# Kernel optimization log

Measured on AMD Instinct MI355X. Metric: run time of the kernel, lower is better.

## Reference

```python
import jax, jax.numpy as jnp
import numpy as np

LN_EPS = 1e-5

def sin_emb(coords, dim):
    # coords [..., 3] -> [..., dim]; dim split evenly over 3 axes, sin/cos halves
    per_axis = dim // 3
    half = per_axis // 2
    freqs = jnp.exp(-jnp.log(10000.0) * jnp.arange(half, dtype=coords.dtype) / max(half - 1, 1))
    ang = coords[..., None] * freqs  # [..., 3, half]
    emb = jnp.concatenate([jnp.sin(ang), jnp.cos(ang)], axis=-1)  # [..., 3, per_axis]
    return emb.reshape(coords.shape[:-1] + (dim,))

def layernorm(x, g, b):
    mu = jnp.mean(x, axis=-1, keepdims=True)
    var = jnp.mean((x - mu) ** 2, axis=-1, keepdims=True)
    return (x - mu) * jax.lax.rsqrt(var + LN_EPS) * g + b

def point_mlp(x, w, b, g, be, act):
    h = layernorm(x @ w + b, g, be)
    return jax.nn.gelu(h, approximate=False) if act else h

def query_ball_point(radius, nsample, xyz):
    # xyz [B,N,3] -> idx [B,N,nsample] (pad with first in-ball index, PointNet++ style)
    N = xyz.shape[1]
    sq = jnp.sum((xyz[:, :, None, :] - xyz[:, None, :, :]) ** 2, axis=-1)  # [B,N,N]
    idx0 = jnp.where(sq > radius * radius, N, jnp.arange(N)[None, None, :])
    idx = jnp.sort(idx0, axis=-1)[:, :, :nsample]
    return jnp.where(idx == N, idx[:, :, :1], idx)

def index_points(points, idx):
    # points [B,N,C], idx [B,S,K] -> [B,S,K,C]
    return jax.vmap(lambda p, i: p[i])(points, idx)

def setup_inputs() -> dict:
    key = jax.random.key(0)
    ks = jax.random.split(key, 20)
    B, N, C_stem, C_tok = 4, 4096, 64, 256
    C_in = C_stem + 3 + 24 + 96  # 187
    w = lambda k, i, o: jax.random.normal(k, (i, o), jnp.float32) * 0.02
    inp = {
        'xyz': jax.random.uniform(ks[0], (B, N, 3), jnp.float32),
        'point_feature': jax.random.normal(ks[1], (B, N, C_stem), jnp.float32),
        # scene_point_mlp
        'w1': w(ks[2], C_in, C_tok), 'b1': jnp.zeros((C_tok,)), 'g1': jnp.ones((C_tok,)), 'be1': jnp.zeros((C_tok,)),
        'w2': w(ks[3], C_tok, C_tok), 'b2': jnp.zeros((C_tok,)), 'g2': jnp.ones((C_tok,)), 'be2': jnp.zeros((C_tok,)),
        # scene_projection
        'pw1': w(ks[4], C_tok, C_tok), 'pb1': jnp.zeros((C_tok,)), 'pg1': jnp.ones((C_tok,)), 'pbe1': jnp.zeros((C_tok,)),
        'pw2': w(ks[5], C_tok, C_tok), 'pb2': jnp.zeros((C_tok,)), 'pg2': jnp.ones((C_tok,)), 'pbe2': jnp.zeros((C_tok,)),
    }
    return inp

def reference(xyz, point_feature, w1, b1, g1, be1, w2, b2, g2, be2,
              pw1, pb1, pg1, pbe1, pw2, pb2, pg2, pbe2):
    radius, K = 0.16, 32
    idx = query_ball_point(radius, K, xyz)                     # [B,N,K]
    grouped_xyz = index_points(xyz, idx)                       # [B,N,K,3]
    grouped_feature = index_points(point_feature, idx)         # [B,N,K,Cs]
    relative_xyz = grouped_xyz - xyz[:, :, None, :]            # [B,N,K,3]
    relative_position = sin_emb(relative_xyz, 24)              # [B,N,K,24]
    absolute_position = sin_emb(xyz, 96)                       # [B,N,96]
    B, N = xyz.shape[0], xyz.shape[1]
    absolute_position = jnp.broadcast_to(absolute_position[:, :, None, :], (B, N, K, 96))
    grouped_input = jnp.concatenate(
        (grouped_feature, relative_xyz, relative_position, absolute_position), axis=-1)
    h = point_mlp(grouped_input, w1, b1, g1, be1, True)
    h = point_mlp(h, w2, b2, g2, be2, False)
    scene_point_feature = jnp.max(h, axis=2)                   # [B,N,C]
    pooled = jnp.max(scene_point_feature, axis=1, keepdims=True)  # [B,1,C]
    t = point_mlp(pooled, pw1, pb1, pg1, pbe1, True)
    global_scene_token = point_mlp(t, pw2, pb2, pg2, pbe2, False)
    return global_scene_token
```

## Files before the change

### kernel.cpp

```cpp
#include <hip/hip_runtime.h>
#include <hip/hip_bf16.h>
#include <math.h>


#define LN_EPS 1e-5f

typedef __attribute__((ext_vector_type(8))) short bf16x8;
typedef __attribute__((ext_vector_type(4))) float f32x4;
typedef __attribute__((ext_vector_type(2))) unsigned int u32x2;
typedef __attribute__((ext_vector_type(4))) unsigned int u32x4;

#if __has_builtin(__builtin_amdgcn_rcpf)
#define FRCP(x) __builtin_amdgcn_rcpf(x)
#else
#define FRCP(x) (1.0f / (x))
#endif

__device__ __forceinline__ unsigned short f2bf(float f) {
    unsigned int x = __float_as_uint(f);
    return (unsigned short)((x + 0x7FFFu + ((x >> 16) & 1u)) >> 16);
}
__device__ __forceinline__ unsigned int pack2(float a, float b) {
    union { __hip_bfloat162 h; unsigned int u; } cvt;
    cvt.h = __float22bfloat162_rn(make_float2(a, b));
    return cvt.u;
}
__device__ __forceinline__ unsigned int fenc(float f) {
    unsigned int u = __float_as_uint(f);
    return (u & 0x80000000u) ? ~u : (u | 0x80000000u);
}
__device__ __forceinline__ float fdec(unsigned int u) {
    return __uint_as_float((u & 0x80000000u) ? (u & 0x7FFFFFFFu) : ~u);
}
__device__ __forceinline__ float gelu_fast(float x) {
    float x2 = x * x;
    float u = x * fmaf(0.0356774081f, x2, 0.7978845608f);
    float e = exp2f(u * -2.8853900818f);
    float r = FRCP(e + 1.0f);
    return x * r;
}
template<int CTRL>
__device__ __forceinline__ float dppadd(float s) {
    int v = __builtin_amdgcn_update_dpp(0, __float_as_int(s), CTRL, 0xF, 0xF, true);
    return s + __int_as_float(v);
}
__device__ __forceinline__ float rowsum16(float x) {
    x = dppadd<0x128>(x);
    x = dppadd<0x124>(x);
    x = dppadd<0x122>(x);
    x = dppadd<0x121>(x);
    return x;
}

__global__ __launch_bounds__(256) void k_prep(
    const float* __restrict__ w1, const float* __restrict__ w2,
    unsigned short* __restrict__ w2T, unsigned short* __restrict__ w1T,
    unsigned int* __restrict__ pooled, int* __restrict__ done)
{
    int t = threadIdx.x, blk = blockIdx.x;
    if (blk < 16) {
        __shared__ unsigned short tile[64][65];
        int tr = blk >> 2, tc = blk & 3;
        #pragma unroll
        for (int rr = 0; rr < 16; ++rr) {
            int kl = rr * 4 + (t >> 6), nl = t & 63;
            tile[kl][nl] = f2bf(w2[(size_t)(tr * 64 + kl) * 256 + tc * 64 + nl]);
        }
        __syncthreads();
        #pragma unroll
        for (int rr = 0; rr < 16; ++rr) {
            int nl = rr * 4 + (t >> 6), kp = t & 63;
            int kl = (kp & 3) * 16 + (kp >> 2);
            w2T[(size_t)(tc * 64 + nl) * 256 + tr * 64 + kp] = tile[kl][nl];
        }
    } else if (blk < 28) {
        __shared__ unsigned short tile[64][65];
        int idx = blk - 16;
        int tr = idx >> 2, tc = idx & 3;
        #pragma unroll
        for (int rr = 0; rr < 16; ++rr) {
            int kl = rr * 4 + (t >> 6), nl = t & 63;
            int kp = tr * 64 + kl;
            float v = 0.f;
            if (kp < 91)                       v = w1[(size_t)kp * 256 + tc * 64 + nl];
            else if (kp >= 92 && kp <= 187)    v = w1[(size_t)(kp - 1) * 256 + tc * 64 + nl];
            tile[kl][nl] = f2bf(v);
        }
        __syncthreads();
        #pragma unroll
        for (int rr = 0; rr < 16; ++rr) {
            int nl = rr * 4 + (t >> 6), kl = t & 63;
            w1T[(size_t)(tc * 64 + nl) * 192 + tr * 64 + kl] = tile[kl][nl];
        }
    } else {
        unsigned int idv = fenc(-1e19f);
        for (int q = t; q < 1024; q += 256) pooled[q] = idv;
        if (t == 0) *done = 0;
    }
}

__global__ __launch_bounds__(256, 4) void k_main(
    const float* __restrict__ xyz, const float* __restrict__ pf,
    const unsigned short* __restrict__ w1T, const unsigned short* __restrict__ w2T,
    const float* __restrict__ b1, const float* __restrict__ g1,
    const float* __restrict__ be1,
    const float* __restrict__ b2, const float* __restrict__ g2,
    const float* __restrict__ be2,
    unsigned int* __restrict__ pooled, int* __restrict__ done,
    const float* __restrict__ pw1, const float* __restrict__ pb1,
    const float* __restrict__ pg1, const float* __restrict__ pbe1,
    const float* __restrict__ pw2, const float* __restrict__ pb2,
    const float* __restrict__ pg2, const float* __restrict__ pbe2,
    float* __restrict__ out)
{
    __shared__ __align__(16) unsigned short smem[64 * 264];
    __shared__ __align__(16) unsigned int epack[2 * 48];
    __shared__ unsigned long long bmask[2][64];
    __shared__ int   idxs[64];
    __shared__ float ctr[2][3];
    __shared__ int   lastf;
    unsigned short* a1s = smem;
    unsigned short* h1s = smem;

    const int N = 4096;
    int tid = threadIdx.x, wv = tid >> 6, lane = tid & 63;
    int lo16 = lane & 15, quad = lane >> 4;
    int b = blockIdx.x & 3;
    int i0 = (blockIdx.x >> 2) * 2;
    size_t base = (size_t)b * N;
    const float* xb = xyz + base * 3;

    bf16x8 bfr0[4], bfr1[4];
    #pragma unroll
    for (int nt = 0; nt < 4; ++nt) {
        int n = wv * 64 + nt * 16 + lo16;
        bfr0[nt] = *(const bf16x8*)&w1T[n * 192 + 0 * 32 + quad * 8];
        bfr1[nt] = *(const bf16x8*)&w1T[n * 192 + 1 * 32 + quad * 8];
    }

    if (tid < 6) { int p = tid / 3, a = tid - 3 * p; ctr[p][a] = xb[(i0 + p) * 3 + a]; }
    if (tid < 96) {
        int p = tid / 48, pr = tid - 48 * p;
        float vals[2];
        #pragma unroll
        for (int q = 0; q < 2; ++q) {
            int cc = pr * 2 + q;
            int a = cc >> 5, wI = cc & 31;
            int jf = (wI < 16) ? wI : (wI - 16);
            float coord = xb[(i0 + p) * 3 + a];
            float fr = __expf(-0.61402269146507894f * (float)jf);
            float ang = coord * fr;
            vals[q] = (wI < 16) ? __sinf(ang) : __cosf(ang);
        }
        epack[p * 48 + pr] = pack2(vals[0], vals[1]);
    }
    const double r2d = 0.16 * 0.16;
    float T = (float)r2d;
    if ((double)T > r2d) T = __uint_as_float(__float_as_uint(T) - 1u);
    {
        float cx0 = xb[i0 * 3], cy0 = xb[i0 * 3 + 1], cz0 = xb[i0 * 3 + 2];
        float cx1 = xb[(i0 + 1) * 3], cy1 = xb[(i0 + 1) * 3 + 1], cz1 = xb[(i0 + 1) * 3 + 2];
        #pragma unroll 4
        for (int i = 0; i < 16; ++i) {
            int chunk = wv * 16 + i;
            int j = chunk * 64 + lane;
            float px = xb[j * 3], py = xb[j * 3 + 1], pz = xb[j * 3 + 2];
            float dx0 = __fsub_rn(px, cx0), dy0 = __fsub_rn(py, cy0), dz0 = __fsub_rn(pz, cz0);
            float sq0 = __fadd_rn(__fadd_rn(__fmul_rn(dx0, dx0), __fmul_rn(dy0, dy0)),
                                  __fmul_rn(dz0, dz0));
            unsigned long long m0 = __ballot(sq0 <= T);
            float dx1 = __fsub_rn(px, cx1), dy1 = __fsub_rn(py, cy1), dz1 = __fsub_rn(pz, cz1);
            float sq1 = __fadd_rn(__fadd_rn(__fmul_rn(dx1, dx1), __fmul_rn(dy1, dy1)),
                                  __fmul_rn(dz1, dz1));
            unsigned long long m1 = __ballot(sq1 <= T);
            if (lane == 0) { bmask[0][chunk] = m0; bmask[1][chunk] = m1; }
        }
    }
    __syncthreads();
    if (wv < 2) {
        int p = wv;
        unsigned long long m = bmask[p][lane];
        int c = __popcll(m);
        int inc = c;
        #pragma unroll
        for (int d = 1; d <= 32; d <<= 1) {
            int v = __shfl_up(inc, d);
            if (lane >= d) inc += v;
        }
        int exc = inc - c;
        int total = __shfl(inc, 63);
        unsigned long long lm = __ballot(m != 0ull);
        int fl = __ffsll(lm) - 1;
        unsigned long long mf = (unsigned long long)__shfl((long long)m, fl);
        int firstj = fl * 64 + __ffsll(mf) - 1;
        unsigned long long mm = m;
        int t = 0;
        while (mm != 0ull && (exc + t) < 32) {
            int bpos = __ffsll(mm) - 1;
            idxs[p * 32 + exc + t] = lane * 64 + bpos;
            mm &= mm - 1; ++t;
        }
        if (lane >= total && lane < 32) idxs[p * 32 + lane] = firstj;
    }
    __syncthreads();

    {
        int r = tid >> 2, seg = tid & 3;
        int j = idxs[r];
        const f32x4* src = (const f32x4*)(pf + (base + (size_t)j) * 64 + seg * 16);
        f32x4 v0 = src[0], v1 = src[1], v2 = src[2], v3 = src[3];
        u32x4 o0, o1;
        o0.x = pack2(v0.x, v0.y); o0.y = pack2(v0.z, v0.w);
        o0.z = pack2(v1.x, v1.y); o0.w = pack2(v1.z, v1.w);
        o1.x = pack2(v2.x, v2.y); o1.y = pack2(v2.z, v2.w);
        o1.z = pack2(v3.x, v3.y); o1.w = pack2(v3.z, v3.w);
        u32x4* dst = (u32x4*)&a1s[r * 200 + seg * 16];
        dst[0] = o0; dst[1] = o1;
    }
    {
        int r = tid & 63, part = tid >> 6;
        int p = r >> 5;
        int j = idxs[r];
        float rx = xb[j * 3]     - ctr[p][0];
        float ry = xb[j * 3 + 1] - ctr[p][1];
        float rz = xb[j * 3 + 2] - ctr[p][2];
        unsigned short* arow = &a1s[r * 200];
        if (part == 0) {
            *(unsigned int*)&arow[64] = pack2(rx, ry);
            arow[66] = f2bf(rz);
            arow[91] = 0;
            *(u32x2*)&arow[188] = (u32x2){0u, 0u};
        } else {
            int a = part - 1;
            float cv = (a == 0) ? rx : ((a == 1) ? ry : rz);
            const float fr4[4] = {1.f, 0.046415888336127774f,
                                  0.0021544346900318843f, 1e-4f};
            float sn[4], cs[4];
            #pragma unroll
            for (int tt = 0; tt < 4; ++tt) {
                float ang = cv * fr4[tt];
                sn[tt] = __sinf(ang); cs[tt] = __cosf(ang);
            }
            arow[67 + a * 8 + 0] = f2bf(sn[0]); arow[67 + a * 8 + 1] = f2bf(sn[1]);
            arow[67 + a * 8 + 2] = f2bf(sn[2]); arow[67 + a * 8 + 3] = f2bf(sn[3]);
            arow[67 + a * 8 + 4] = f2bf(cs[0]); arow[67 + a * 8 + 5] = f2bf(cs[1]);
            arow[67 + a * 8 + 6] = f2bf(cs[2]); arow[67 + a * 8 + 7] = f2bf(cs[3]);
        }
    }
    {
        int r = tid >> 2, part = tid & 3, p = r >> 5;
        const u32x2* e = (const u32x2*)(epack + p * 48 + part * 12);
        u32x2* dst = (u32x2*)&a1s[r * 200 + 92 + part * 24];
        #pragma unroll
        for (int q = 0; q < 6; ++q) dst[q] = e[q];
    }
    __syncthreads();

    f32x4 acc[4][4];
    {
        float b1f[4];
        #pragma unroll
        for (int nt = 0; nt < 4; ++nt) b1f[nt] = b1[wv * 64 + nt * 16 + lo16];
        #pragma unroll
        for (int mt = 0; mt < 4; ++mt)
            #pragma unroll
            for (int nt = 0; nt < 4; ++nt)
                #pragma unroll
                for (int reg = 0; reg < 4; ++reg) acc[mt][nt][reg] = b1f[nt];
    }
    #pragma unroll
    for (int mt = 0; mt < 4; ++mt) {
        bf16x8 afr = *(const bf16x8*)&a1s[(mt * 16 + lo16) * 200 + 0 * 32 + quad * 8];
        #pragma unroll
        for (int nt = 0; nt < 4; ++nt)
            acc[mt][nt] = __builtin_amdgcn_mfma_f32_16x16x32_bf16(
                afr, bfr0[nt], acc[mt][nt], 0, 0, 0);
    }
    #pragma unroll
    for (int mt = 0; mt < 4; ++mt) {
        bf16x8 afr = *(const bf16x8*)&a1s[(mt * 16 + lo16) * 200 + 1 * 32 + quad * 8];
        #pragma unroll
        for (int nt = 0; nt < 4; ++nt)
            acc[mt][nt] = __builtin_amdgcn_mfma_f32_16x16x32_bf16(
                afr, bfr1[nt], acc[mt][nt], 0, 0, 0);
    }
    for (int ks = 2; ks < 6; ++ks) {
        bf16x8 bfr[4];
        #pragma unroll
        for (int nt = 0; nt < 4; ++nt) {
            int n = wv * 64 + nt * 16 + lo16;
            bfr[nt] = *(const bf16x8*)&w1T[n * 192 + ks * 32 + quad * 8];
        }
        #pragma unroll
        for (int mt = 0; mt < 4; ++mt) {
            bf16x8 afr = *(const bf16x8*)&a1s[(mt * 16 + lo16) * 200 + ks * 32 + quad * 8];
            #pragma unroll
            for (int nt = 0; nt < 4; ++nt)
                acc[mt][nt] = __builtin_amdgcn_mfma_f32_16x16x32_bf16(
                    afr, bfr[nt], acc[mt][nt], 0, 0, 0);
        }
    }

    __shared__ float reds[64][4][2];
    __shared__ float musig[64][2];
    #pragma unroll
    for (int mt = 0; mt < 4; ++mt) {
        #pragma unroll
        for (int reg = 0; reg < 4; ++reg) {
            float s1 = 0.f, s2 = 0.f;
            #pragma unroll
            for (int nt = 0; nt < 4; ++nt) { float v = acc[mt][nt][reg]; s1 += v; s2 = fmaf(v, v, s2); }
            s1 = rowsum16(s1); s2 = rowsum16(s2);
            if (lo16 == 0) { int r = mt * 16 + quad * 4 + reg; reds[r][wv][0] = s1; reds[r][wv][1] = s2; }
        }
    }
    __syncthreads();
    if (tid < 64) {
        int r = tid;
        float s1 = reds[r][0][0] + reds[r][1][0] + reds[r][2][0] + reds[r][3][0];
        float s2 = reds[r][0][1] + reds[r][1][1] + reds[r][2][1] + reds[r][3][1];
        float mu = s1 * (1.f / 256.f);
        float var = fmaxf(s2 * (1.f / 256.f) - mu * mu, 0.f);
        musig[r][0] = mu; musig[r][1] = rsqrtf(var + LN_EPS);
    }
    __syncthreads();
    {
        float g1f[4], be1f[4];
        #pragma unroll
        for (int nt = 0; nt < 4; ++nt) {
            int n = wv * 64 + nt * 16 + lo16;
            g1f[nt] = g1[n]; be1f[nt] = be1[n];
        }
        #pragma unroll
        for (int mt = 0; mt < 4; ++mt) {
            #pragma unroll
            for (int reg = 0; reg < 4; ++reg) {
                int r = mt * 16 + quad * 4 + reg;
                float mu = musig[r][0], rs = musig[r][1];
                float v0 = gelu_fast(fmaf((acc[mt][0][reg] - mu) * rs, g1f[0], be1f[0]));
                float v1 = gelu_fast(fmaf((acc[mt][1][reg] - mu) * rs, g1f[1], be1f[1]));
                float v2 = gelu_fast(fmaf((acc[mt][2][reg] - mu) * rs, g1f[2], be1f[2]));
                float v3 = gelu_fast(fmaf((acc[mt][3][reg] - mu) * rs, g1f[3], be1f[3]));
                u32x2 w; w.x = pack2(v0, v1); w.y = pack2(v2, v3);
                *(u32x2*)&h1s[r * 264 + wv * 64 + lo16 * 4] = w;
            }
        }
    }
    __syncthreads();

    {
        float b2f[4];
        #pragma unroll
        for (int nt = 0; nt < 4; ++nt) b2f[nt] = b2[wv * 64 + nt * 16 + lo16];
        #pragma unroll
        for (int mt = 0; mt < 4; ++mt)
            #pragma unroll
            for (int nt = 0; nt < 4; ++nt)
                #pragma unroll
                for (int reg = 0; reg < 4; ++reg) acc[mt][nt][reg] = b2f[nt];
    }
    for (int ks = 0; ks < 8; ++ks) {
        bf16x8 bfr[4], afr[4];
        #pragma unroll
        for (int nt = 0; nt < 4; ++nt) {
            int n = wv * 64 + nt * 16 + lo16;
            bfr[nt] = *(const bf16x8*)&w2T[n * 256 + ks * 32 + quad * 8];
        }
        #pragma unroll
        for (int mt = 0; mt < 4; ++mt)
            afr[mt] = *(const bf16x8*)&h1s[(mt * 16 + lo16) * 264 + ks * 32 + quad * 8];
        #pragma unroll
        for (int mt = 0; mt < 4; ++mt)
            #pragma unroll
            for (int nt = 0; nt < 4; ++nt)
                acc[mt][nt] = __builtin_amdgcn_mfma_f32_16x16x32_bf16(
                    afr[mt], bfr[nt], acc[mt][nt], 0, 0, 0);
    }

    {
        #pragma unroll
        for (int mt = 0; mt < 4; ++mt) {
            #pragma unroll
            for (int reg = 0; reg < 4; ++reg) {
                float s1 = 0.f, s2 = 0.f;
                #pragma unroll
                for (int nt = 0; nt < 4; ++nt) { float v = acc[mt][nt][reg]; s1 += v; s2 = fmaf(v, v, s2); }
                s1 = rowsum16(s1); s2 = rowsum16(s2);
                if (lo16 == 0) { int r = mt * 16 + quad * 4 + reg; reds[r][wv][0] = s1; reds[r][wv][1] = s2; }
            }
        }
        __syncthreads();
        if (tid < 64) {
            int r = tid;
            float s1 = reds[r][0][0] + reds[r][1][0] + reds[r][2][0] + reds[r][3][0];
            float s2 = reds[r][0][1] + reds[r][1][1] + reds[r][2][1] + reds[r][3][1];
            float mu = s1 * (1.f / 256.f);
            float var = fmaxf(s2 * (1.f / 256.f) - mu * mu, 0.f);
            musig[r][0] = mu; musig[r][1] = rsqrtf(var + LN_EPS);
        }
        __syncthreads();

        float g2f[4], be2f[4];
        #pragma unroll
        for (int nt = 0; nt < 4; ++nt) {
            int n = wv * 64 + nt * 16 + lo16;
            g2f[nt] = g2[n]; be2f[nt] = be2[n];
        }
        float mx[4] = {-1e30f, -1e30f, -1e30f, -1e30f};
        #pragma unroll
        for (int mt = 0; mt < 4; ++mt) {
            #pragma unroll
            for (int reg = 0; reg < 4; ++reg) {
                int r = mt * 16 + quad * 4 + reg;
                float mu = musig[r][0], rs = musig[r][1];
                #pragma unroll
                for (int nt = 0; nt < 4; ++nt) {
                    float v = fmaf((acc[mt][nt][reg] - mu) * rs, g2f[nt], be2f[nt]);
                    mx[nt] = fmaxf(mx[nt], v);
                }
            }
        }
        #pragma unroll
        for (int nt = 0; nt < 4; ++nt) {
            mx[nt] = fmaxf(mx[nt], __shfl_xor(mx[nt], 16));
            mx[nt] = fmaxf(mx[nt], __shfl_xor(mx[nt], 32));
        }
        if (quad == 0) {
            #pragma unroll
            for (int nt = 0; nt < 4; ++nt)
                atomicMax(pooled + b * 256 + wv * 64 + nt * 16 + lo16, fenc(mx[nt]));
        }
    }

    __syncthreads();
    if (tid == 0) lastf = (atomicAdd(done, 1) == 8191);
    __syncthreads();
    if (!lastf) return;
    {
        int bb = wv;
        float* xw = (float*)smem + wv * 512;
        #pragma unroll
        for (int q = 0; q < 4; ++q)
            xw[q * 64 + lane] =
                fdec(atomicMax(&pooled[bb * 256 + q * 64 + lane], 0u));

        float a1[4];
        #pragma unroll
        for (int q = 0; q < 4; ++q) a1[q] = pb1[q * 64 + lane];
        #pragma unroll 4
        for (int k = 0; k < 256; ++k) {
            float xv = xw[k];
            const float* wr = pw1 + (size_t)k * 256 + lane;
            #pragma unroll
            for (int q = 0; q < 4; ++q) a1[q] = fmaf(xv, wr[q * 64], a1[q]);
        }
        float s1 = a1[0] + a1[1] + a1[2] + a1[3];
        float s2 = fmaf(a1[0], a1[0], fmaf(a1[1], a1[1],
                   fmaf(a1[2], a1[2], a1[3] * a1[3])));
        s1 = rowsum16(s1); s2 = rowsum16(s2);
        s1 += __shfl_xor(s1, 16); s2 += __shfl_xor(s2, 16);
        s1 += __shfl_xor(s1, 32); s2 += __shfl_xor(s2, 32);
        float mu = s1 * (1.f / 256.f);
        float rs = rsqrtf(fmaxf(s2 * (1.f / 256.f) - mu * mu, 0.f) + LN_EPS);
        #pragma unroll
        for (int q = 0; q < 4; ++q) {
            int c = q * 64 + lane;
            xw[256 + c] = gelu_fast(fmaf((a1[q] - mu) * rs, pg1[c], pbe1[c]));
        }

        float a2[4];
        #pragma unroll
        for (int q = 0; q < 4; ++q) a2[q] = pb2[q * 64 + lane];
        #pragma unroll 4
        for (int k = 0; k < 256; ++k) {
            float xv = xw[256 + k];
            const float* wr = pw2 + (size_t)k * 256 + lane;
            #pragma unroll
            for (int q = 0; q < 4; ++q) a2[q] = fmaf(xv, wr[q * 64], a2[q]);
        }
        s1 = a2[0] + a2[1] + a2[2] + a2[3];
        s2 = fmaf(a2[0], a2[0], fmaf(a2[1], a2[1],
             fmaf(a2[2], a2[2], a2[3] * a2[3])));
        s1 = rowsum16(s1); s2 = rowsum16(s2);
        s1 += __shfl_xor(s1, 16); s2 += __shfl_xor(s2, 16);
        s1 += __shfl_xor(s1, 32); s2 += __shfl_xor(s2, 32);
        mu = s1 * (1.f / 256.f);
        rs = rsqrtf(fmaxf(s2 * (1.f / 256.f) - mu * mu, 0.f) + LN_EPS);
        #pragma unroll
        for (int q = 0; q < 4; ++q) {
            int c = q * 64 + lane;
            out[bb * 256 + c] = fmaf((a2[q] - mu) * rs, pg2[c], pbe2[c]);
        }
    }
}

extern "C" void kernel_launch(void* const* d_in, const int* in_sizes, int n_in,
                              void* d_out, int out_size, void* d_ws, size_t ws_size,
                              hipStream_t stream)
{
    char* ws = (char*)d_ws;
    unsigned short* w2T    = (unsigned short*)ws;
    unsigned short* w1T    = (unsigned short*)(ws + (128u << 10));
    unsigned int*   pooled = (unsigned int*)(ws + (224u << 10));
    int*            done   = (int*)(ws + (228u << 10));

    k_prep<<<29, 256, 0, stream>>>((const float*)d_in[2], (const float*)d_in[6],
                                   w2T, w1T, pooled, done);
    k_main<<<8192, 256, 0, stream>>>((const float*)d_in[0], (const float*)d_in[1],
                                     w1T, w2T,
                                     (const float*)d_in[3], (const float*)d_in[4],
                                     (const float*)d_in[5],
                                     (const float*)d_in[7], (const float*)d_in[8],
                                     (const float*)d_in[9], pooled, done,
                                     (const float*)d_in[10], (const float*)d_in[11],
                                     (const float*)d_in[12], (const float*)d_in[13],
                                     (const float*)d_in[14], (const float*)d_in[15],
                                     (const float*)d_in[16], (const float*)d_in[17],
                                     (float*)d_out);
}
```

Baseline: 418.9 us.

## Process four centers per block with 512 threads and a 2x4 wave grid

Each block now handles four query points (128 grouped rows) with 8 waves arranged as 2 M-groups by 4 N-groups, halving the grid to 4096 blocks. The ball query computes four ballots per loaded point, and center coordinates are read with vector loads. Fewer blocks means fewer repeated weight-fragment loads, fewer per-block setup scans over all 4096 points, and fewer atomics per center. The cost is that shared memory roughly doubles to about 70KB per block, which limits occupancy, and the per-block scan still reads every point for only four centers.

```diff
diff --git a/kernel.cpp b/kernel.cpp
--- a/kernel.cpp
+++ b/kernel.cpp
@@ -99,7 +99,7 @@
     }
 }
 
-__global__ __launch_bounds__(256, 4) void k_main(
+__global__ __launch_bounds__(512, 4) void k_main(
     const float* __restrict__ xyz, const float* __restrict__ pf,
     const unsigned short* __restrict__ w1T, const unsigned short* __restrict__ w2T,
     const float* __restrict__ b1, const float* __restrict__ g1,
@@ -113,11 +113,11 @@
     const float* __restrict__ pg2, const float* __restrict__ pbe2,
     float* __restrict__ out)
 {
-    __shared__ __align__(16) unsigned short smem[64 * 264];
-    __shared__ __align__(16) unsigned int epack[2 * 48];
-    __shared__ unsigned long long bmask[2][64];
-    __shared__ int   idxs[64];
-    __shared__ float ctr[2][3];
+    __shared__ __align__(16) unsigned short smem[128 * 264];
+    __shared__ __align__(16) unsigned int epack[4 * 48];
+    __shared__ unsigned long long bmask[4][64];
+    __shared__ int   idxs[128];
+    __shared__ float ctr[4][3];
     __shared__ int   lastf;
     unsigned short* a1s = smem;
     unsigned short* h1s = smem;
@@ -125,21 +125,21 @@
     const int N = 4096;
     int tid = threadIdx.x, wv = tid >> 6, lane = tid & 63;
     int lo16 = lane & 15, quad = lane >> 4;
+    int wvM = wv >> 2, wvN = wv & 3;
     int b = blockIdx.x & 3;
-    int i0 = (blockIdx.x >> 2) * 2;
+    int i0 = (blockIdx.x >> 2) * 4;
     size_t base = (size_t)b * N;
     const float* xb = xyz + base * 3;
 
-    bf16x8 bfr0[4], bfr1[4];
+    bf16x8 bfr0[4];
     #pragma unroll
     for (int nt = 0; nt < 4; ++nt) {
-        int n = wv * 64 + nt * 16 + lo16;
+        int n = wvN * 64 + nt * 16 + lo16;
         bfr0[nt] = *(const bf16x8*)&w1T[n * 192 + 0 * 32 + quad * 8];
-        bfr1[nt] = *(const bf16x8*)&w1T[n * 192 + 1 * 32 + quad * 8];
-    }
-
-    if (tid < 6) { int p = tid / 3, a = tid - 3 * p; ctr[p][a] = xb[(i0 + p) * 3 + a]; }
-    if (tid < 96) {
+    }
+
+    if (tid < 12) { int p = tid / 3, a = tid - 3 * p; ctr[p][a] = xb[(i0 + p) * 3 + a]; }
+    if (tid < 192) {
         int p = tid / 48, pr = tid - 48 * p;
         float vals[2];
         #pragma unroll
@@ -158,13 +158,19 @@
     float T = (float)r2d;
     if ((double)T > r2d) T = __uint_as_float(__float_as_uint(T) - 1u);
     {
-        float cx0 = xb[i0 * 3], cy0 = xb[i0 * 3 + 1], cz0 = xb[i0 * 3 + 2];
-        float cx1 = xb[(i0 + 1) * 3], cy1 = xb[(i0 + 1) * 3 + 1], cz1 = xb[(i0 + 1) * 3 + 2];
-        #pragma unroll 4
-        for (int i = 0; i < 16; ++i) {
-            int chunk = wv * 16 + i;
+        f32x4 cA = *(const f32x4*)(xb + (size_t)i0 * 3);
+        f32x4 cB = *(const f32x4*)(xb + (size_t)i0 * 3 + 4);
+        f32x4 cC = *(const f32x4*)(xb + (size_t)i0 * 3 + 8);
+        float cx0 = cA.x, cy0 = cA.y, cz0 = cA.z;
+        float cx1 = cA.w, cy1 = cB.x, cz1 = cB.y;
+        float cx2 = cB.z, cy2 = cB.w, cz2 = cC.x;
+        float cx3 = cC.y, cy3 = cC.z, cz3 = cC.w;
+        #pragma unroll 2
+        for (int i = 0; i < 8; ++i) {
+            int chunk = wv * 8 + i;
             int j = chunk * 64 + lane;
-            float px = xb[j * 3], py = xb[j * 3 + 1], pz = xb[j * 3 + 2];
+            const float* pp = xb + (size_t)j * 3;
+            float px = pp[0], py = pp[1], pz = pp[2];
             float dx0 = __fsub_rn(px, cx0), dy0 = __fsub_rn(py, cy0), dz0 = __fsub_rn(pz, cz0);
             float sq0 = __fadd_rn(__fadd_rn(__fmul_rn(dx0, dx0), __fmul_rn(dy0, dy0)),
                                   __fmul_rn(dz0, dz0));
@@ -173,11 +179,22 @@
             float sq1 = __fadd_rn(__fadd_rn(__fmul_rn(dx1, dx1), __fmul_rn(dy1, dy1)),
                                   __fmul_rn(dz1, dz1));
             unsigned long long m1 = __ballot(sq1 <= T);
-            if (lane == 0) { bmask[0][chunk] = m0; bmask[1][chunk] = m1; }
-        }
-    }
-    __syncthreads();
-    if (wv < 2) {
+            float dx2 = __fsub_rn(px, cx2), dy2 = __fsub_rn(py, cy2), dz2 = __fsub_rn(pz, cz2);
+            float sq2 = __fadd_rn(__fadd_rn(__fmul_rn(dx2, dx2), __fmul_rn(dy2, dy2)),
+                                  __fmul_rn(dz2, dz2));
+            unsigned long long m2 = __ballot(sq2 <= T);
+            float dx3 = __fsub_rn(px, cx3), dy3 = __fsub_rn(py, cy3), dz3 = __fsub_rn(pz, cz3);
+            float sq3 = __fadd_rn(__fadd_rn(__fmul_rn(dx3, dx3), __fmul_rn(dy3, dy3)),
+                                  __fmul_rn(dz3, dz3));
+            unsigned long long m3 = __ballot(sq3 <= T);
+            if (lane == 0) {
+                bmask[0][chunk] = m0; bmask[1][chunk] = m1;
+                bmask[2][chunk] = m2; bmask[3][chunk] = m3;
+            }
+        }
+    }
+    __syncthreads();
+    if (wv < 4) {
         int p = wv;
         unsigned long long m = bmask[p][lane];
         int c = __popcll(m);
@@ -218,7 +235,7 @@
         dst[0] = o0; dst[1] = o1;
     }
     {
-        int r = tid & 63, part = tid >> 6;
+        int r = tid & 127, part = tid >> 7;
         int p = r >> 5;
         int j = idxs[r];
         float rx = xb[j * 3]     - ctr[p][0];
@@ -254,13 +271,20 @@
         #pragma unroll
         for (int q = 0; q < 6; ++q) dst[q] = e[q];
     }
-    __syncthreads();
-
+    bf16x8 bfr1[4];
+    #pragma unroll
+    for (int nt = 0; nt < 4; ++nt) {
+        int n = wvN * 64 + nt * 16 + lo16;
+        bfr1[nt] = *(const bf16x8*)&w1T[n * 192 + 1 * 32 + quad * 8];
+    }
+    __syncthreads();
+
+    const int arow0 = wvM * 64;
     f32x4 acc[4][4];
     {
         float b1f[4];
         #pragma unroll
-        for (int nt = 0; nt < 4; ++nt) b1f[nt] = b1[wv * 64 + nt * 16 + lo16];
+        for (int nt = 0; nt < 4; ++nt) b1f[nt] = b1[wvN * 64 + nt * 16 + lo16];
         #pragma unroll
         for (int mt = 0; mt < 4; ++mt)
             #pragma unroll
@@ -270,7 +294,7 @@
     }
     #pragma unroll
     for (int mt = 0; mt < 4; ++mt) {
-        bf16x8 afr = *(const bf16x8*)&a1s[(mt * 16 + lo16) * 200 + 0 * 32 + quad * 8];
+        bf16x8 afr = *(const bf16x8*)&a1s[(arow0 + mt * 16 + lo16) * 200 + 0 * 32 + quad * 8];
         #pragma unroll
         for (int nt = 0; nt < 4; ++nt)
             acc[mt][nt] = __builtin_amdgcn_mfma_f32_16x16x32_bf16(
@@ -278,7 +302,7 @@
     }
     #pragma unroll
     for (int mt = 0; mt < 4; ++mt) {
-        bf16x8 afr = *(const bf16x8*)&a1s[(mt * 16 + lo16) * 200 + 1 * 32 + quad * 8];
+        bf16x8 afr = *(const bf16x8*)&a1s[(arow0 + mt * 16 + lo16) * 200 + 1 * 32 + quad * 8];
         #pragma unroll
         for (int nt = 0; nt < 4; ++nt)
             acc[mt][nt] = __builtin_amdgcn_mfma_f32_16x16x32_bf16(
@@ -288,12 +312,12 @@
         bf16x8 bfr[4];
         #pragma unroll
         for (int nt = 0; nt < 4; ++nt) {
-            int n = wv * 64 + nt * 16 + lo16;
+            int n = wvN * 64 + nt * 16 + lo16;
             bfr[nt] = *(const bf16x8*)&w1T[n * 192 + ks * 32 + quad * 8];
         }
         #pragma unroll
         for (int mt = 0; mt < 4; ++mt) {
-            bf16x8 afr = *(const bf16x8*)&a1s[(mt * 16 + lo16) * 200 + ks * 32 + quad * 8];
+            bf16x8 afr = *(const bf16x8*)&a1s[(arow0 + mt * 16 + lo16) * 200 + ks * 32 + quad * 8];
             #pragma unroll
             for (int nt = 0; nt < 4; ++nt)
                 acc[mt][nt] = __builtin_amdgcn_mfma_f32_16x16x32_bf16(
@@ -301,8 +325,8 @@
         }
     }
 
-    __shared__ float reds[64][4][2];
-    __shared__ float musig[64][2];
+    __shared__ float reds[128][4][2];
+    __shared__ float musig[128][2];
     #pragma unroll
     for (int mt = 0; mt < 4; ++mt) {
         #pragma unroll
@@ -311,11 +335,14 @@
             #pragma unroll
             for (int nt = 0; nt < 4; ++nt) { float v = acc[mt][nt][reg]; s1 += v; s2 = fmaf(v, v, s2); }
             s1 = rowsum16(s1); s2 = rowsum16(s2);
-            if (lo16 == 0) { int r = mt * 16 + quad * 4 + reg; reds[r][wv][0] = s1; reds[r][wv][1] = s2; }
-        }
-    }
-    __syncthreads();
-    if (tid < 64) {
+            if (lo16 == 0) {
+                int r = arow0 + mt * 16 + quad * 4 + reg;
+                reds[r][wvN][0] = s1; reds[r][wvN][1] = s2;
+            }
+        }
+    }
+    __syncthreads();
+    if (tid < 128) {
         int r = tid;
         float s1 = reds[r][0][0] + reds[r][1][0] + reds[r][2][0] + reds[r][3][0];
         float s2 = reds[r][0][1] + reds[r][1][1] + reds[r][2][1] + reds[r][3][1];
@@ -328,21 +355,21 @@
         float g1f[4], be1f[4];
         #pragma unroll
         for (int nt = 0; nt < 4; ++nt) {
-            int n = wv * 64 + nt * 16 + lo16;
+            int n = wvN * 64 + nt * 16 + lo16;
             g1f[nt] = g1[n]; be1f[nt] = be1[n];
         }
         #pragma unroll
         for (int mt = 0; mt < 4; ++mt) {
             #pragma unroll
             for (int reg = 0; reg < 4; ++reg) {
-                int r = mt * 16 + quad * 4 + reg;
+                int r = arow0 + mt * 16 + quad * 4 + reg;
                 float mu = musig[r][0], rs = musig[r][1];
                 float v0 = gelu_fast(fmaf((acc[mt][0][reg] - mu) * rs, g1f[0], be1f[0]));
                 float v1 = gelu_fast(fmaf((acc[mt][1][reg] - mu) * rs, g1f[1], be1f[1]));
                 float v2 = gelu_fast(fmaf((acc[mt][2][reg] - mu) * rs, g1f[2], be1f[2]));
                 float v3 = gelu_fast(fmaf((acc[mt][3][reg] - mu) * rs, g1f[3], be1f[3]));
                 u32x2 w; w.x = pack2(v0, v1); w.y = pack2(v2, v3);
-                *(u32x2*)&h1s[r * 264 + wv * 64 + lo16 * 4] = w;
+                *(u32x2*)&h1s[r * 264 + wvN * 64 + lo16 * 4] = w;
             }
         }
     }
@@ -351,7 +378,7 @@
     {
         float b2f[4];
         #pragma unroll
-        for (int nt = 0; nt < 4; ++nt) b2f[nt] = b2[wv * 64 + nt * 16 + lo16];
+        for (int nt = 0; nt < 4; ++nt) b2f[nt] = b2[wvN * 64 + nt * 16 + lo16];
         #pragma unroll
         for (int mt = 0; mt < 4; ++mt)
             #pragma unroll
@@ -363,12 +390,12 @@
         bf16x8 bfr[4], afr[4];
         #pragma unroll
         for (int nt = 0; nt < 4; ++nt) {
-            int n = wv * 64 + nt * 16 + lo16;
+            int n = wvN * 64 + nt * 16 + lo16;
             bfr[nt] = *(const bf16x8*)&w2T[n * 256 + ks * 32 + quad * 8];
         }
         #pragma unroll
         for (int mt = 0; mt < 4; ++mt)
-            afr[mt] = *(const bf16x8*)&h1s[(mt * 16 + lo16) * 264 + ks * 32 + quad * 8];
+            afr[mt] = *(const bf16x8*)&h1s[(arow0 + mt * 16 + lo16) * 264 + ks * 32 + quad * 8];
         #pragma unroll
         for (int mt = 0; mt < 4; ++mt)
             #pragma unroll
@@ -386,11 +413,14 @@
                 #pragma unroll
                 for (int nt = 0; nt < 4; ++nt) { float v = acc[mt][nt][reg]; s1 += v; s2 = fmaf(v, v, s2); }
                 s1 = rowsum16(s1); s2 = rowsum16(s2);
-                if (lo16 == 0) { int r = mt * 16 + quad * 4 + reg; reds[r][wv][0] = s1; reds[r][wv][1] = s2; }
+                if (lo16 == 0) {
+                    int r = arow0 + mt * 16 + quad * 4 + reg;
+                    reds[r][wvN][0] = s1; reds[r][wvN][1] = s2;
+                }
             }
         }
         __syncthreads();
-        if (tid < 64) {
+        if (tid < 128) {
             int r = tid;
             float s1 = reds[r][0][0] + reds[r][1][0] + reds[r][2][0] + reds[r][3][0];
             float s2 = reds[r][0][1] + reds[r][1][1] + reds[r][2][1] + reds[r][3][1];
@@ -403,7 +433,7 @@
         float g2f[4], be2f[4];
         #pragma unroll
         for (int nt = 0; nt < 4; ++nt) {
-            int n = wv * 64 + nt * 16 + lo16;
+            int n = wvN * 64 + nt * 16 + lo16;
             g2f[nt] = g2[n]; be2f[nt] = be2[n];
         }
         float mx[4] = {-1e30f, -1e30f, -1e30f, -1e30f};
@@ -411,7 +441,7 @@
         for (int mt = 0; mt < 4; ++mt) {
             #pragma unroll
             for (int reg = 0; reg < 4; ++reg) {
-                int r = mt * 16 + quad * 4 + reg;
+                int r = arow0 + mt * 16 + quad * 4 + reg;
                 float mu = musig[r][0], rs = musig[r][1];
                 #pragma unroll
                 for (int nt = 0; nt < 4; ++nt) {
@@ -428,15 +458,15 @@
         if (quad == 0) {
             #pragma unroll
             for (int nt = 0; nt < 4; ++nt)
-                atomicMax(pooled + b * 256 + wv * 64 + nt * 16 + lo16, fenc(mx[nt]));
-        }
-    }
-
-    __syncthreads();
-    if (tid == 0) lastf = (atomicAdd(done, 1) == 8191);
+                atomicMax(pooled + b * 256 + wvN * 64 + nt * 16 + lo16, fenc(mx[nt]));
+        }
+    }
+
+    __syncthreads();
+    if (tid == 0) lastf = (atomicAdd(done, 1) == 4095);
     __syncthreads();
     if (!lastf) return;
-    {
+    if (wv < 4) {
         int bb = wv;
         float* xw = (float*)smem + wv * 512;
         #pragma unroll
@@ -506,7 +536,7 @@
 
     k_prep<<<29, 256, 0, stream>>>((const float*)d_in[2], (const float*)d_in[6],
                                    w2T, w1T, pooled, done);
-    k_main<<<8192, 256, 0, stream>>>((const float*)d_in[0], (const float*)d_in[1],
+    k_main<<<4096, 512, 0, stream>>>((const float*)d_in[0], (const float*)d_in[1],
                                      w1T, w2T,
                                      (const float*)d_in[3], (const float*)d_in[4],
                                      (const float*)d_in[5],
```

Result: slower. 444.0 us (+6.0%).

## Split per-block MLP work across 16 waves with 2x8 wave tiling

Applied to the files above, without the earlier changes.

Raises the block to 1024 threads and tiles both MLP GEMMs as 2 row-groups by 8 column-groups of waves, each computing a 32x32 output tile. The ball query, gather and embedding stages are spread across more waves, and the LayerNorm reductions now combine eight partial sums. The w2T K-permutation is changed to match the new h1s packing. This aims to cut per-thread register pressure and serial work per block, at the cost of less register reuse of weight fragments and more costly block-wide barriers.

```diff
diff --git a/kernel.cpp b/kernel.cpp
--- a/kernel.cpp
+++ b/kernel.cpp
@@ -70,7 +70,8 @@
         #pragma unroll
         for (int rr = 0; rr < 16; ++rr) {
             int nl = rr * 4 + (t >> 6), kp = t & 63;
-            int kl = (kp & 3) * 16 + (kp >> 2);
+            int g = kp >> 5, w = kp & 31;
+            int kl = g * 32 + (w & 1) * 16 + (w >> 1);
             w2T[(size_t)(tc * 64 + nl) * 256 + tr * 64 + kp] = tile[kl][nl];
         }
     } else if (blk < 28) {
@@ -99,7 +100,7 @@
     }
 }
 
-__global__ __launch_bounds__(256, 4) void k_main(
+__global__ __launch_bounds__(1024, 8) void k_main(
     const float* __restrict__ xyz, const float* __restrict__ pf,
     const unsigned short* __restrict__ w1T, const unsigned short* __restrict__ w2T,
     const float* __restrict__ b1, const float* __restrict__ g1,
@@ -118,6 +119,8 @@
     __shared__ unsigned long long bmask[2][64];
     __shared__ int   idxs[64];
     __shared__ float ctr[2][3];
+    __shared__ float reds[64][8][2];
+    __shared__ float musig[64][2];
     __shared__ int   lastf;
     unsigned short* a1s = smem;
     unsigned short* h1s = smem;
@@ -125,18 +128,11 @@
     const int N = 4096;
     int tid = threadIdx.x, wv = tid >> 6, lane = tid & 63;
     int lo16 = lane & 15, quad = lane >> 4;
+    int wvM = wv >> 3, wvN = wv & 7;
     int b = blockIdx.x & 3;
     int i0 = (blockIdx.x >> 2) * 2;
     size_t base = (size_t)b * N;
     const float* xb = xyz + base * 3;
-
-    bf16x8 bfr0[4], bfr1[4];
-    #pragma unroll
-    for (int nt = 0; nt < 4; ++nt) {
-        int n = wv * 64 + nt * 16 + lo16;
-        bfr0[nt] = *(const bf16x8*)&w1T[n * 192 + 0 * 32 + quad * 8];
-        bfr1[nt] = *(const bf16x8*)&w1T[n * 192 + 1 * 32 + quad * 8];
-    }
 
     if (tid < 6) { int p = tid / 3, a = tid - 3 * p; ctr[p][a] = xb[(i0 + p) * 3 + a]; }
     if (tid < 96) {
@@ -160,11 +156,12 @@
     {
         float cx0 = xb[i0 * 3], cy0 = xb[i0 * 3 + 1], cz0 = xb[i0 * 3 + 2];
         float cx1 = xb[(i0 + 1) * 3], cy1 = xb[(i0 + 1) * 3 + 1], cz1 = xb[(i0 + 1) * 3 + 2];
-        #pragma unroll 4
-        for (int i = 0; i < 16; ++i) {
-            int chunk = wv * 16 + i;
+        #pragma unroll 2
+        for (int i = 0; i < 4; ++i) {
+            int chunk = wv * 4 + i;
             int j = chunk * 64 + lane;
-            float px = xb[j * 3], py = xb[j * 3 + 1], pz = xb[j * 3 + 2];
+            const float* pp = xb + (size_t)j * 3;
+            float px = pp[0], py = pp[1], pz = pp[2];
             float dx0 = __fsub_rn(px, cx0), dy0 = __fsub_rn(py, cy0), dz0 = __fsub_rn(pz, cz0);
             float sq0 = __fadd_rn(__fadd_rn(__fmul_rn(dx0, dx0), __fmul_rn(dy0, dy0)),
                                   __fmul_rn(dz0, dz0));
@@ -204,7 +201,7 @@
     }
     __syncthreads();
 
-    {
+    if (tid < 256) {
         int r = tid >> 2, seg = tid & 3;
         int j = idxs[r];
         const f32x4* src = (const f32x4*)(pf + (base + (size_t)j) * 64 + seg * 16);
@@ -217,8 +214,9 @@
         u32x4* dst = (u32x4*)&a1s[r * 200 + seg * 16];
         dst[0] = o0; dst[1] = o1;
     }
-    {
-        int r = tid & 63, part = tid >> 6;
+    else if (tid < 512) {
+        int t2 = tid - 256;
+        int r = t2 & 63, part = t2 >> 6;
         int p = r >> 5;
         int j = idxs[r];
         float rx = xb[j * 3]     - ctr[p][0];
@@ -247,8 +245,9 @@
             arow[67 + a * 8 + 6] = f2bf(cs[2]); arow[67 + a * 8 + 7] = f2bf(cs[3]);
         }
     }
-    {
-        int r = tid >> 2, part = tid & 3, p = r >> 5;
+    else if (tid < 768) {
+        int t2 = tid - 512;
+        int r = t2 >> 2, part = t2 & 3, p = r >> 5;
         const u32x2* e = (const u32x2*)(epack + p * 48 + part * 12);
         u32x2* dst = (u32x2*)&a1s[r * 200 + 92 + part * 24];
         #pragma unroll
@@ -256,179 +255,167 @@
     }
     __syncthreads();
 
-    f32x4 acc[4][4];
+    const int arow0 = wvM * 32;
+    f32x4 acc[2][2];
     {
-        float b1f[4];
-        #pragma unroll
-        for (int nt = 0; nt < 4; ++nt) b1f[nt] = b1[wv * 64 + nt * 16 + lo16];
-        #pragma unroll
-        for (int mt = 0; mt < 4; ++mt)
-            #pragma unroll
-            for (int nt = 0; nt < 4; ++nt)
+        float b1f[2];
+        #pragma unroll
+        for (int nt = 0; nt < 2; ++nt) b1f[nt] = b1[wvN * 32 + nt * 16 + lo16];
+        #pragma unroll
+        for (int mt = 0; mt < 2; ++mt)
+            #pragma unroll
+            for (int nt = 0; nt < 2; ++nt)
                 #pragma unroll
                 for (int reg = 0; reg < 4; ++reg) acc[mt][nt][reg] = b1f[nt];
     }
-    #pragma unroll
-    for (int mt = 0; mt < 4; ++mt) {
-        bf16x8 afr = *(const bf16x8*)&a1s[(mt * 16 + lo16) * 200 + 0 * 32 + quad * 8];
-        #pragma unroll
-        for (int nt = 0; nt < 4; ++nt)
-            acc[mt][nt] = __builtin_amdgcn_mfma_f32_16x16x32_bf16(
-                afr, bfr0[nt], acc[mt][nt], 0, 0, 0);
-    }
-    #pragma unroll
-    for (int mt = 0; mt < 4; ++mt) {
-        bf16x8 afr = *(const bf16x8*)&a1s[(mt * 16 + lo16) * 200 + 1 * 32 + quad * 8];
-        #pragma unroll
-        for (int nt = 0; nt < 4; ++nt)
-            acc[mt][nt] = __builtin_amdgcn_mfma_f32_16x16x32_bf16(
-                afr, bfr1[nt], acc[mt][nt], 0, 0, 0);
-    }
-    for (int ks = 2; ks < 6; ++ks) {
-        bf16x8 bfr[4];
-        #pragma unroll
-        for (int nt = 0; nt < 4; ++nt) {
-            int n = wv * 64 + nt * 16 + lo16;
+    for (int ks = 0; ks < 6; ++ks) {
+        bf16x8 bfr[2];
+        #pragma unroll
+        for (int nt = 0; nt < 2; ++nt) {
+            int n = wvN * 32 + nt * 16 + lo16;
             bfr[nt] = *(const bf16x8*)&w1T[n * 192 + ks * 32 + quad * 8];
         }
         #pragma unroll
-        for (int mt = 0; mt < 4; ++mt) {
-            bf16x8 afr = *(const bf16x8*)&a1s[(mt * 16 + lo16) * 200 + ks * 32 + quad * 8];
-            #pragma unroll
-            for (int nt = 0; nt < 4; ++nt)
+        for (int mt = 0; mt < 2; ++mt) {
+            bf16x8 afr = *(const bf16x8*)&a1s[(arow0 + mt * 16 + lo16) * 200 + ks * 32 + quad * 8];
+            #pragma unroll
+            for (int nt = 0; nt < 2; ++nt)
                 acc[mt][nt] = __builtin_amdgcn_mfma_f32_16x16x32_bf16(
                     afr, bfr[nt], acc[mt][nt], 0, 0, 0);
         }
     }
 
-    __shared__ float reds[64][4][2];
-    __shared__ float musig[64][2];
     #pragma unroll
-    for (int mt = 0; mt < 4; ++mt) {
+    for (int mt = 0; mt < 2; ++mt) {
         #pragma unroll
         for (int reg = 0; reg < 4; ++reg) {
             float s1 = 0.f, s2 = 0.f;
             #pragma unroll
-            for (int nt = 0; nt < 4; ++nt) { float v = acc[mt][nt][reg]; s1 += v; s2 = fmaf(v, v, s2); }
+            for (int nt = 0; nt < 2; ++nt) { float v = acc[mt][nt][reg]; s1 += v; s2 = fmaf(v, v, s2); }
             s1 = rowsum16(s1); s2 = rowsum16(s2);
-            if (lo16 == 0) { int r = mt * 16 + quad * 4 + reg; reds[r][wv][0] = s1; reds[r][wv][1] = s2; }
+            if (lo16 == 0) {
+                int r = arow0 + mt * 16 + quad * 4 + reg;
+                reds[r][wvN][0] = s1; reds[r][wvN][1] = s2;
+            }
         }
     }
     __syncthreads();
     if (tid < 64) {
         int r = tid;
-        float s1 = reds[r][0][0] + reds[r][1][0] + reds[r][2][0] + reds[r][3][0];
-        float s2 = reds[r][0][1] + reds[r][1][1] + reds[r][2][1] + reds[r][3][1];
+        float s1 = 0.f, s2 = 0.f;
+        #pragma unroll
+        for (int g = 0; g < 8; ++g) { s1 += reds[r][g][0]; s2 += reds[r][g][1]; }
         float mu = s1 * (1.f / 256.f);
         float var = fmaxf(s2 * (1.f / 256.f) - mu * mu, 0.f);
         musig[r][0] = mu; musig[r][1] = rsqrtf(var + LN_EPS);
     }
     __syncthreads();
     {
-        float g1f[4], be1f[4];
-        #pragma unroll
-        for (int nt = 0; nt < 4; ++nt) {
-            int n = wv * 64 + nt * 16 + lo16;
+        float g1f[2], be1f[2];
+        #pragma unroll
+        for (int nt = 0; nt < 2; ++nt) {
+            int n = wvN * 32 + nt * 16 + lo16;
             g1f[nt] = g1[n]; be1f[nt] = be1[n];
         }
         #pragma unroll
-        for (int mt = 0; mt < 4; ++mt) {
+        for (int mt = 0; mt < 2; ++mt) {
             #pragma unroll
             for (int reg = 0; reg < 4; ++reg) {
-                int r = mt * 16 + quad * 4 + reg;
+                int r = arow0 + mt * 16 + quad * 4 + reg;
                 float mu = musig[r][0], rs = musig[r][1];
                 float v0 = gelu_fast(fmaf((acc[mt][0][reg] - mu) * rs, g1f[0], be1f[0]));
                 float v1 = gelu_fast(fmaf((acc[mt][1][reg] - mu) * rs, g1f[1], be1f[1]));
-                float v2 = gelu_fast(fmaf((acc[mt][2][reg] - mu) * rs, g1f[2], be1f[2]));
-                float v3 = gelu_fast(fmaf((acc[mt][3][reg] - mu) * rs, g1f[3], be1f[3]));
-                u32x2 w; w.x = pack2(v0, v1); w.y = pack2(v2, v3);
-                *(u32x2*)&h1s[r * 264 + wv * 64 + lo16 * 4] = w;
+                *(unsigned int*)&h1s[r * 264 + wvN * 32 + lo16 * 2] = pack2(v0, v1);
             }
         }
     }
     __syncthreads();
 
     {
-        float b2f[4];
-        #pragma unroll
-        for (int nt = 0; nt < 4; ++nt) b2f[nt] = b2[wv * 64 + nt * 16 + lo16];
-        #pragma unroll
-        for (int mt = 0; mt < 4; ++mt)
-            #pragma unroll
-            for (int nt = 0; nt < 4; ++nt)
+        float b2f[2];
+        #pragma unroll
+        for (int nt = 0; nt < 2; ++nt) b2f[nt] = b2[wvN * 32 + nt * 16 + lo16];
+        #pragma unroll
+        for (int mt = 0; mt < 2; ++mt)
+            #pragma unroll
+            for (int nt = 0; nt < 2; ++nt)
                 #pragma unroll
                 for (int reg = 0; reg < 4; ++reg) acc[mt][nt][reg] = b2f[nt];
     }
     for (int ks = 0; ks < 8; ++ks) {
-        bf16x8 bfr[4], afr[4];
-        #pragma unroll
-        for (int nt = 0; nt < 4; ++nt) {
-            int n = wv * 64 + nt * 16 + lo16;
+        bf16x8 bfr[2], afr[2];
+        #pragma unroll
+        for (int nt = 0; nt < 2; ++nt) {
+            int n = wvN * 32 + nt * 16 + lo16;
             bfr[nt] = *(const bf16x8*)&w2T[n * 256 + ks * 32 + quad * 8];
         }
         #pragma unroll
-        for (int mt = 0; mt < 4; ++mt)
-            afr[mt] = *(const bf16x8*)&h1s[(mt * 16 + lo16) * 264 + ks * 32 + quad * 8];
-        #pragma unroll
-        for (int mt = 0; mt < 4; ++mt)
-            #pragma unroll
-            for (int nt = 0; nt < 4; ++nt)
+        for (int mt = 0; mt < 2; ++mt)
+            afr[mt] = *(const bf16x8*)&h1s[(arow0 + mt * 16 + lo16) * 264 + ks * 32 + quad * 8];
+        #pragma unroll
+        for (int mt = 0; mt < 2; ++mt)
+            #pragma unroll
+            for (int nt = 0; nt < 2; ++nt)
                 acc[mt][nt] = __builtin_amdgcn_mfma_f32_16x16x32_bf16(
                     afr[mt], bfr[nt], acc[mt][nt], 0, 0, 0);
     }
 
     {
         #pragma unroll
-        for (int mt = 0; mt < 4; ++mt) {
+        for (int mt = 0; mt < 2; ++mt) {
             #pragma unroll
             for (int reg = 0; reg < 4; ++reg) {
                 float s1 = 0.f, s2 = 0.f;
                 #pragma unroll
-                for (int nt = 0; nt < 4; ++nt) { float v = acc[mt][nt][reg]; s1 += v; s2 = fmaf(v, v, s2); }
+                for (int nt = 0; nt < 2; ++nt) { float v = acc[mt][nt][reg]; s1 += v; s2 = fmaf(v, v, s2); }
                 s1 = rowsum16(s1); s2 = rowsum16(s2);
-                if (lo16 == 0) { int r = mt * 16 + quad * 4 + reg; reds[r][wv][0] = s1; reds[r][wv][1] = s2; }
+                if (lo16 == 0) {
+                    int r = arow0 + mt * 16 + quad * 4 + reg;
+                    reds[r][wvN][0] = s1; reds[r][wvN][1] = s2;
+                }
             }
         }
         __syncthreads();
         if (tid < 64) {
             int r = tid;
-            float s1 = reds[r][0][0] + reds[r][1][0] + reds[r][2][0] + reds[r][3][0];
-            float s2 = reds[r][0][1] + reds[r][1][1] + reds[r][2][1] + reds[r][3][1];
+            float s1 = 0.f, s2 = 0.f;
+            #pragma unroll
+            for (int g = 0; g < 8; ++g) { s1 += reds[r][g][0]; s2 += reds[r][g][1]; }
             float mu = s1 * (1.f / 256.f);
             float var = fmaxf(s2 * (1.f / 256.f) - mu * mu, 0.f);
             musig[r][0] = mu; musig[r][1] = rsqrtf(var + LN_EPS);
         }
         __syncthreads();
 
-        float g2f[4], be2f[4];
-        #pragma unroll
-        for (int nt = 0; nt < 4; ++nt) {
-            int n = wv * 64 + nt * 16 + lo16;
+        float g2f[2], be2f[2];
+        #pragma unroll
+        for (int nt = 0; nt < 2; ++nt) {
+            int n = wvN * 32 + nt * 16 + lo16;
             g2f[nt] = g2[n]; be2f[nt] = be2[n];
         }
-        float mx[4] = {-1e30f, -1e30f, -1e30f, -1e30f};
-        #pragma unroll
-        for (int mt = 0; mt < 4; ++mt) {
+        float mx[2] = {-1e30f, -1e30f};
+        #pragma unroll
+        for (int mt = 0; mt < 2; ++mt) {
             #pragma unroll
             for (int reg = 0; reg < 4; ++reg) {
-                int r = mt * 16 + quad * 4 + reg;
+                int r = arow0 + mt * 16 + quad * 4 + reg;
                 float mu = musig[r][0], rs = musig[r][1];
                 #pragma unroll
-                for (int nt = 0; nt < 4; ++nt) {
+                for (int nt = 0; nt < 2; ++nt) {
                     float v = fmaf((acc[mt][nt][reg] - mu) * rs, g2f[nt], be2f[nt]);
                     mx[nt] = fmaxf(mx[nt], v);
                 }
             }
         }
         #pragma unroll
-        for (int nt = 0; nt < 4; ++nt) {
+        for (int nt = 0; nt < 2; ++nt) {
             mx[nt] = fmaxf(mx[nt], __shfl_xor(mx[nt], 16));
             mx[nt] = fmaxf(mx[nt], __shfl_xor(mx[nt], 32));
         }
         if (quad == 0) {
             #pragma unroll
-            for (int nt = 0; nt < 4; ++nt)
-                atomicMax(pooled + b * 256 + wv * 64 + nt * 16 + lo16, fenc(mx[nt]));
+            for (int nt = 0; nt < 2; ++nt)
+                atomicMax(pooled + b * 256 + wvN * 32 + nt * 16 + lo16, fenc(mx[nt]));
         }
     }
 
@@ -436,7 +423,7 @@
     if (tid == 0) lastf = (atomicAdd(done, 1) == 8191);
     __syncthreads();
     if (!lastf) return;
-    {
+    if (wv < 4) {
         int bb = wv;
         float* xw = (float*)smem + wv * 512;
         #pragma unroll
@@ -506,15 +493,15 @@
 
     k_prep<<<29, 256, 0, stream>>>((const float*)d_in[2], (const float*)d_in[6],
                                    w2T, w1T, pooled, done);
-    k_main<<<8192, 256, 0, stream>>>((const float*)d_in[0], (const float*)d_in[1],
-                                     w1T, w2T,
-                                     (const float*)d_in[3], (const float*)d_in[4],
-                                     (const float*)d_in[5],
-                                     (const float*)d_in[7], (const float*)d_in[8],
-                                     (const float*)d_in[9], pooled, done,
-                                     (const float*)d_in[10], (const float*)d_in[11],
-                                     (const float*)d_in[12], (const float*)d_in[13],
-                                     (const float*)d_in[14], (const float*)d_in[15],
-                                     (const float*)d_in[16], (const float*)d_in[17],
-                                     (float*)d_out);
-}
+    k_main<<<8192, 1024, 0, stream>>>((const float*)d_in[0], (const float*)d_in[1],
+                                      w1T, w2T,
+                                      (const float*)d_in[3], (const float*)d_in[4],
+                                      (const float*)d_in[5],
+                                      (const float*)d_in[7], (const float*)d_in[8],
+                                      (const float*)d_in[9], pooled, done,
+                                      (const float*)d_in[10], (const float*)d_in[11],
+                                      (const float*)d_in[12], (const float*)d_in[13],
+                                      (const float*)d_in[14], (const float*)d_in[15],
+                                      (const float*)d_in[16], (const float*)d_in[17],
+                                      (float*)d_out);
+}
```

Result: slower. 634.8 us (+51.6%).
